# Kernel optimization log

Measured on AMD Instinct MI355X. Metric: run time of the kernel, lower is better.

## Reference

```python
import jax, jax.numpy as jnp
import numpy as np

B, H, S, D = 4, 16, 2048, 64
SQRT_D = float(D) ** 0.5
NEG = -1000000000.0


def setup_inputs() -> dict:
    key = jax.random.key(0)
    kq, kk, kv = jax.random.split(key, 3)
    q = jax.random.normal(kq, (B, H, S, D), dtype=jnp.float32)
    k = jax.random.normal(kk, (B, H, S, D), dtype=jnp.float32)
    v = jax.random.normal(kv, (B, H, S, D), dtype=jnp.float32)
    # causal mask: 1 where attention allowed, 0 where blocked (code masks where mask==0)
    mask = jnp.tril(jnp.ones((S, S), dtype=jnp.int32))[None, None]  # [1,1,S,S]
    return {"q": q, "k": k, "v": v, "mask": mask}


def reference(q, k, v, mask):
    # score: [B,H,S,S]
    score = jnp.einsum("bhqd,bhkd->bhqk", q, k) / SQRT_D
    score = jnp.where(mask == 0, NEG, score)
    attn_weights = jax.nn.softmax(score, axis=-1)
    # dropout p=0.0 -> identity
    attention_output = jnp.einsum("bhqk,bhkd->bhqd", attn_weights, v)
    return (attention_output, attn_weights)
```

## Files before the change

### kernel.cpp

```cpp
#include <hip/hip_runtime.h>
#include <hip/hip_bf16.h>

#define B_ 4
#define H_ 16
#define S_ 2048
#define D_ 64
#define QBLK 128
#define NQB 16
#define THREADS 512

typedef float  f32x4  __attribute__((ext_vector_type(4)));
typedef short  bf16x8 __attribute__((ext_vector_type(8)));
typedef unsigned uint2v __attribute__((ext_vector_type(2)));

#define LOG2E_O8  0.18033688011112042f
#define M20LOG2E -28.853900817779268f

__device__ __forceinline__ unsigned cvt_pk(float lo, float hi) {
    unsigned r;
    asm("v_cvt_pk_bf16_f32 %0, %1, %2" : "=v"(r) : "v"(lo), "v"(hi));
    return r;
}

__device__ __forceinline__ void nt_store4(float* p, f32x4 v) {
    __builtin_nontemporal_store(v, (f32x4*)p);
}

__device__ __forceinline__ void bar_lds() {
    asm volatile("s_waitcnt lgkmcnt(0)\n\ts_barrier" ::: "memory");
}

__device__ __forceinline__ int swz(int row, int s8) {
    return row * 8 + (s8 ^ ((row & 7) ^ ((row >> 3) & 7)));
}

__device__ __forceinline__ bf16x8 frag_ld(const short* lds, int row, int s8) {
    return *(const bf16x8*)((const char*)lds + 16 * swz(row, s8));
}

__device__ __forceinline__ void kload(f32x4 (&r)[2], const float* __restrict__ g, int t) {
    r[0] = *(const f32x4*)(g + 4 * t);
    r[1] = *(const f32x4*)(g + 4 * (t + THREADS));
}
__device__ __forceinline__ void kwrite(short* lds, const f32x4 (&r)[2], int t) {
#pragma unroll
    for (int i = 0; i < 2; ++i) {
        int f = t + i * THREADS;
        int row = f >> 4, c4 = f & 15;
        uint2v h;
        h.x = cvt_pk(r[i].x, r[i].y);
        h.y = cvt_pk(r[i].z, r[i].w);
        *(uint2v*)((char*)lds + 16 * swz(row, c4 >> 1) + (c4 & 1) * 8) = h;
    }
}
__device__ __forceinline__ void vload(f32x4 (&r)[2], const float* __restrict__ g, int t) {
    int k0 = (t >> 4) * 2, d0 = (t & 15) * 4;
    r[0] = *(const f32x4*)(g + k0 * 64 + d0);
    r[1] = *(const f32x4*)(g + (k0 + 1) * 64 + d0);
}
__device__ __forceinline__ void vtwrite(short* lds, const f32x4 (&r)[2], int t) {
    int k0 = (t >> 4) * 2, d0 = (t & 15) * 4;
#pragma unroll
    for (int j = 0; j < 4; ++j) {
        unsigned pk = cvt_pk(r[0][j], r[1][j]);
        int row = d0 + j;
        *(unsigned*)((char*)lds + 16 * swz(row, k0 >> 3) + (k0 & 7) * 2) = pk;
    }
}

__global__ __launch_bounds__(THREADS)
void attn_kernel(const float* __restrict__ Q, const float* __restrict__ K,
                 const float* __restrict__ V, float* __restrict__ Out) {
    const int t    = threadIdx.x;
    const int lane = t & 63;
    const int w    = t >> 6;
    const int l15  = lane & 15;
    const int l4   = lane >> 4;

    const int bid = blockIdx.x;
    const int u   = bid >> 3;
    const int qbi = (NQB - 1) - ((u + 4 * (u >> 5)) & (NQB - 1));
    const int bh  = (bid & 7) * 8 + (u >> 4);
    const int q0  = qbi * QBLK;

    const float* Qg = Q + ((size_t)bh * S_ + q0) * D_;
    const float* Kg = K + (size_t)bh * S_ * D_;
    const float* Vg = V + (size_t)bh * S_ * D_;
    float* Og = Out + ((size_t)bh * S_ + q0) * D_;
    float* Wg = Out + (size_t)B_ * H_ * S_ * D_ + ((size_t)bh * S_ + q0) * (size_t)S_;

    __shared__ char pool[40960];
    short* lkb = (short*)pool;
    short* lv  = (short*)(pool + 16384);
    short* lp  = (short*)(pool + 24576) + w * 1024;

    {
        f32x4 z = {0.f, 0.f, 0.f, 0.f};
        for (int row = 0; row < QBLK; ++row) {
            int c0 = q0 + (row & ~63) + 64;
            float* p = Wg + (size_t)row * S_;
            for (int c = c0 + 4 * t; c < S_; c += 4 * THREADS)
                nt_store4(p + c, z);
        }
    }

    bf16x8 qa0, qa1;
    {
        const float* qrow = Qg + (size_t)(16 * w + l15) * D_;
        f32x4 a0 = *(const f32x4*)(qrow + 8 * l4);
        f32x4 a1 = *(const f32x4*)(qrow + 8 * l4 + 4);
        f32x4 b0 = *(const f32x4*)(qrow + 32 + 8 * l4);
        f32x4 b1 = *(const f32x4*)(qrow + 32 + 8 * l4 + 4);
        union { bf16x8 v; unsigned u[4]; } q0u, q1u;
        q0u.u[0] = cvt_pk(a0.x, a0.y); q0u.u[1] = cvt_pk(a0.z, a0.w);
        q0u.u[2] = cvt_pk(a1.x, a1.y); q0u.u[3] = cvt_pk(a1.z, a1.w);
        q1u.u[0] = cvt_pk(b0.x, b0.y); q1u.u[1] = cvt_pk(b0.z, b0.w);
        q1u.u[2] = cvt_pk(b1.x, b1.y); q1u.u[3] = cvt_pk(b1.z, b1.w);
        qa0 = q0u.v; qa1 = q1u.v;
    }

    const int ktmax  = (q0 + QBLK - 1) >> 6;
    const int qwbase = q0 + 16 * w;
    const int qg     = qwbase + l15;

    f32x4 kreg[2];
    kload(kreg, Kg, t);
    kwrite(lkb, kreg, t);
    kload(kreg, Kg + 4096, t);
    bar_lds();

    f32x4 lsum4 = {0.f, 0.f, 0.f, 0.f};
    for (int kt = 0; kt <= ktmax; ++kt) {
        const short* lk = lkb + (kt & 1) * 4096;
#pragma unroll
        for (int kc = 0; kc < 4; ++kc) {
            int kgb = kt * 64 + 16 * kc;
            if (kgb > qwbase) break;
            bf16x8 kb0 = frag_ld(lk, 16 * kc + l15, 0 + l4);
            bf16x8 kb1 = frag_ld(lk, 16 * kc + l15, 4 + l4);
            f32x4 acc = {0.f, 0.f, 0.f, 0.f};
            acc = __builtin_amdgcn_mfma_f32_16x16x32_bf16(kb0, qa0, acc, 0, 0, 0);
            acc = __builtin_amdgcn_mfma_f32_16x16x32_bf16(kb1, qa1, acc, 0, 0, 0);
            if (kgb != qwbase) {
#pragma unroll
                for (int r = 0; r < 4; ++r)
                    lsum4[r] += exp2f(fmaf(acc[r], LOG2E_O8, M20LOG2E));
            } else {
#pragma unroll
                for (int r = 0; r < 4; ++r) {
                    int kg = kgb + 4 * l4 + r;
                    if (kg <= qg) lsum4[r] += exp2f(fmaf(acc[r], LOG2E_O8, M20LOG2E));
                }
            }
        }
        if (kt < ktmax) {
            kwrite(lkb + ((kt + 1) & 1) * 4096, kreg, t);
            if (kt + 1 < ktmax) kload(kreg, Kg + (size_t)(kt + 2) * 4096, t);
        }
        bar_lds();
    }
    float lsum = (lsum4[0] + lsum4[1]) + (lsum4[2] + lsum4[3]);
    lsum += __shfl_xor(lsum, 16);
    lsum += __shfl_xor(lsum, 32);
    const float c2 = M20LOG2E - __log2f(lsum);

    f32x4 oacc[4];
#pragma unroll
    for (int dt = 0; dt < 4; ++dt) oacc[dt] = (f32x4){0.f, 0.f, 0.f, 0.f};

    f32x4 vreg[2];
    kload(kreg, Kg, t);
    vload(vreg, Vg, t);
    kwrite(lkb, kreg, t);
    vtwrite(lv, vreg, t);
    kload(kreg, Kg + 4096, t);
    vload(vreg, Vg + 4096, t);
    bar_lds();

    for (int kt = 0; kt <= ktmax; ++kt) {
        const short* lk = lkb + (kt & 1) * 4096;
        const bool blive = (kt * 64 <= qwbase);

        if (blive) {
#pragma unroll
            for (int kc = 0; kc < 4; ++kc) {
                int kgb = kt * 64 + 16 * kc;
                bool live = (kgb <= qwbase);
                f32x4 wv;
                if (live) {
                    bf16x8 kb0 = frag_ld(lk, 16 * kc + l15, 0 + l4);
                    bf16x8 kb1 = frag_ld(lk, 16 * kc + l15, 4 + l4);
                    f32x4 acc = {0.f, 0.f, 0.f, 0.f};
                    acc = __builtin_amdgcn_mfma_f32_16x16x32_bf16(kb0, qa0, acc, 0, 0, 0);
                    acc = __builtin_amdgcn_mfma_f32_16x16x32_bf16(kb1, qa1, acc, 0, 0, 0);
                    if (kgb != qwbase) {
#pragma unroll
                        for (int r = 0; r < 4; ++r)
                            wv[r] = exp2f(fmaf(acc[r], LOG2E_O8, c2));
                    } else {
#pragma unroll
                        for (int r = 0; r < 4; ++r) {
                            int kg = kgb + 4 * l4 + r;
                            wv[r] = (kg <= qg) ? exp2f(fmaf(acc[r], LOG2E_O8, c2)) : 0.0f;
                        }
                    }
                } else {
                    wv = (f32x4){0.f, 0.f, 0.f, 0.f};
                }
                uint2v pk;
                pk.x = cvt_pk(wv[0], wv[1]);
                pk.y = cvt_pk(wv[2], wv[3]);
                int s8 = 2 * kc + (l4 >> 1);
                *(uint2v*)((char*)lp + 16 * swz(l15, s8) + (l4 & 1) * 8) = pk;
            }
#pragma unroll
            for (int j = 0; j < 4; ++j) {
                int rr = j * 4 + l4;
                uint2v pk = *(const uint2v*)((char*)lp + 16 * swz(rr, l15 >> 1) + (l15 & 1) * 8);
                f32x4 wf;
                wf.x = __uint_as_float(pk.x << 16);
                wf.y = __uint_as_float(pk.x & 0xffff0000u);
                wf.z = __uint_as_float(pk.y << 16);
                wf.w = __uint_as_float(pk.y & 0xffff0000u);
                nt_store4(Wg + (size_t)(16 * w + rr) * S_ + kt * 64 + 4 * l15, wf);
            }
        }

        if (kt < ktmax) {
            kwrite(lkb + ((kt + 1) & 1) * 4096, kreg, t);
            if (kt + 1 < ktmax) kload(kreg, Kg + (size_t)(kt + 2) * 4096, t);
        }

        if (blive) {
#pragma unroll
            for (int kchunk = 0; kchunk < 2; ++kchunk) {
                bf16x8 pa = frag_ld(lp, l15, kchunk * 4 + l4);
#pragma unroll
                for (int dt = 0; dt < 4; ++dt) {
                    bf16x8 vb = frag_ld(lv, 16 * dt + l15, kchunk * 4 + l4);
                    oacc[dt] = __builtin_amdgcn_mfma_f32_16x16x32_bf16(pa, vb, oacc[dt], 0, 0, 0);
                }
            }
        }
        bar_lds();
        if (kt < ktmax) {
            vtwrite(lv, vreg, t);
            if (kt + 1 < ktmax) vload(vreg, Vg + (size_t)(kt + 2) * 4096, t);
        }
        bar_lds();
    }

#pragma unroll
    for (int dt = 0; dt < 4; ++dt)
#pragma unroll
        for (int r = 0; r < 4; ++r)
            Og[(size_t)(16 * w + 4 * l4 + r) * D_ + 16 * dt + l15] = oacc[dt][r];
}

extern "C" void kernel_launch(void* const* d_in, const int* in_sizes, int n_in,
                              void* d_out, int out_size, void* d_ws, size_t ws_size,
                              hipStream_t stream) {
    const float* q = (const float*)d_in[0];
    const float* k = (const float*)d_in[1];
    const float* v = (const float*)d_in[2];
    float* out = (float*)d_out;
    attn_kernel<<<dim3(B_ * H_ * NQB), dim3(THREADS), 0, stream>>>(q, k, v, out);
}
```

Baseline: 257.9 us.

## Pair complementary causal query tiles per block and interleave zero-fill stores

Each block now handles two 64-row query tiles, a and 31-a, one per group of four waves, so every block carries the same causal workload and the triangular imbalance across blocks goes away. The up-front zero-fill of the masked upper region of the attention-weight matrix is replaced by a quota of zero stores spread over the first-pass key-tile iterations, so those writes overlap with compute. The cost is that the low tile's waves sit through b+1 iterations with most of them idle, and there is more address arithmetic in the fill loop.

```diff
diff --git a/kernel.cpp b/kernel.cpp
--- a/kernel.cpp
+++ b/kernel.cpp
@@ -5,8 +5,6 @@
 #define H_ 16
 #define S_ 2048
 #define D_ 64
-#define QBLK 128
-#define NQB 16
 #define THREADS 512
 
 typedef float  f32x4  __attribute__((ext_vector_type(4)));
@@ -74,39 +72,31 @@
     const int t    = threadIdx.x;
     const int lane = t & 63;
     const int w    = t >> 6;
+    const int wg   = w & 3;
+    const int grp  = w >> 2;
     const int l15  = lane & 15;
     const int l4   = lane >> 4;
 
     const int bid = blockIdx.x;
     const int u   = bid >> 3;
-    const int qbi = (NQB - 1) - ((u + 4 * (u >> 5)) & (NQB - 1));
     const int bh  = (bid & 7) * 8 + (u >> 4);
-    const int q0  = qbi * QBLK;
-
-    const float* Qg = Q + ((size_t)bh * S_ + q0) * D_;
+    const int a   = u & 15;
+    const int b   = 31 - a;
+    const int q0  = (grp ? b : a) * 64;
+
     const float* Kg = K + (size_t)bh * S_ * D_;
     const float* Vg = V + (size_t)bh * S_ * D_;
-    float* Og = Out + ((size_t)bh * S_ + q0) * D_;
-    float* Wg = Out + (size_t)B_ * H_ * S_ * D_ + ((size_t)bh * S_ + q0) * (size_t)S_;
+    float* Wh = Out + (size_t)B_ * H_ * S_ * D_ + (size_t)bh * S_ * (size_t)S_;
+    float* Oh = Out + (size_t)bh * S_ * D_;
 
     __shared__ char pool[40960];
     short* lkb = (short*)pool;
     short* lv  = (short*)(pool + 16384);
     short* lp  = (short*)(pool + 24576) + w * 1024;
 
-    {
-        f32x4 z = {0.f, 0.f, 0.f, 0.f};
-        for (int row = 0; row < QBLK; ++row) {
-            int c0 = q0 + (row & ~63) + 64;
-            float* p = Wg + (size_t)row * S_;
-            for (int c = c0 + 4 * t; c < S_; c += 4 * THREADS)
-                nt_store4(p + c, z);
-        }
-    }
-
     bf16x8 qa0, qa1;
     {
-        const float* qrow = Qg + (size_t)(16 * w + l15) * D_;
+        const float* qrow = Q + ((size_t)bh * S_ + q0 + 16 * wg + l15) * D_;
         f32x4 a0 = *(const f32x4*)(qrow + 8 * l4);
         f32x4 a1 = *(const f32x4*)(qrow + 8 * l4 + 4);
         f32x4 b0 = *(const f32x4*)(qrow + 32 + 8 * l4);
@@ -119,8 +109,7 @@
         qa0 = q0u.v; qa1 = q1u.v;
     }
 
-    const int ktmax  = (q0 + QBLK - 1) >> 6;
-    const int qwbase = q0 + 16 * w;
+    const int qwbase = q0 + 16 * wg;
     const int qg     = qwbase + l15;
 
     f32x4 kreg[2];
@@ -129,33 +118,49 @@
     kload(kreg, Kg + 4096, t);
     bar_lds();
 
+    int fcur = 0;
+    const int fquota = (62 + b) / (b + 1);
+    const f32x4 z4 = {0.f, 0.f, 0.f, 0.f};
+    const int frow = t >> 4, fcol = 4 * (t & 15);
+
     f32x4 lsum4 = {0.f, 0.f, 0.f, 0.f};
-    for (int kt = 0; kt <= ktmax; ++kt) {
+    for (int kt = 0; kt <= b; ++kt) {
         const short* lk = lkb + (kt & 1) * 4096;
-#pragma unroll
-        for (int kc = 0; kc < 4; ++kc) {
-            int kgb = kt * 64 + 16 * kc;
-            if (kgb > qwbase) break;
-            bf16x8 kb0 = frag_ld(lk, 16 * kc + l15, 0 + l4);
-            bf16x8 kb1 = frag_ld(lk, 16 * kc + l15, 4 + l4);
-            f32x4 acc = {0.f, 0.f, 0.f, 0.f};
-            acc = __builtin_amdgcn_mfma_f32_16x16x32_bf16(kb0, qa0, acc, 0, 0, 0);
-            acc = __builtin_amdgcn_mfma_f32_16x16x32_bf16(kb1, qa1, acc, 0, 0, 0);
-            if (kgb != qwbase) {
-#pragma unroll
-                for (int r = 0; r < 4; ++r)
-                    lsum4[r] += exp2f(fmaf(acc[r], LOG2E_O8, M20LOG2E));
-            } else {
-#pragma unroll
-                for (int r = 0; r < 4; ++r) {
-                    int kg = kgb + 4 * l4 + r;
-                    if (kg <= qg) lsum4[r] += exp2f(fmaf(acc[r], LOG2E_O8, M20LOG2E));
+        if (kt * 64 <= qwbase) {
+#pragma unroll
+            for (int kc = 0; kc < 4; ++kc) {
+                int kgb = kt * 64 + 16 * kc;
+                if (kgb > qwbase) break;
+                bf16x8 kb0 = frag_ld(lk, 16 * kc + l15, 0 + l4);
+                bf16x8 kb1 = frag_ld(lk, 16 * kc + l15, 4 + l4);
+                f32x4 acc = {0.f, 0.f, 0.f, 0.f};
+                acc = __builtin_amdgcn_mfma_f32_16x16x32_bf16(kb0, qa0, acc, 0, 0, 0);
+                acc = __builtin_amdgcn_mfma_f32_16x16x32_bf16(kb1, qa1, acc, 0, 0, 0);
+                if (kgb != qwbase) {
+#pragma unroll
+                    for (int r = 0; r < 4; ++r)
+                        lsum4[r] += exp2f(fmaf(acc[r], LOG2E_O8, M20LOG2E));
+                } else {
+#pragma unroll
+                    for (int r = 0; r < 4; ++r) {
+                        int kg = kgb + 4 * l4 + r;
+                        if (kg <= qg) lsum4[r] += exp2f(fmaf(acc[r], LOG2E_O8, M20LOG2E));
+                    }
                 }
             }
         }
-        if (kt < ktmax) {
+        for (int f = 0; f < fquota; ++f) {
+            if (fcur >= 62) break;
+            int zt = fcur >> 1, half = fcur & 1;
+            int rowb, ktile;
+            if (zt < b) { rowb = 64 * a; ktile = a + 1 + zt; }
+            else        { rowb = 64 * b; ktile = zt + 1; }
+            nt_store4(Wh + (size_t)(rowb + 32 * half + frow) * S_ + 64 * ktile + fcol, z4);
+            ++fcur;
+        }
+        if (kt < b) {
             kwrite(lkb + ((kt + 1) & 1) * 4096, kreg, t);
-            if (kt + 1 < ktmax) kload(kreg, Kg + (size_t)(kt + 2) * 4096, t);
+            if (kt + 1 < b) kload(kreg, Kg + (size_t)(kt + 2) * 4096, t);
         }
         bar_lds();
     }
@@ -177,7 +182,7 @@
     vload(vreg, Vg + 4096, t);
     bar_lds();
 
-    for (int kt = 0; kt <= ktmax; ++kt) {
+    for (int kt = 0; kt <= b; ++kt) {
         const short* lk = lkb + (kt & 1) * 4096;
         const bool blive = (kt * 64 <= qwbase);
 
@@ -222,13 +227,13 @@
                 wf.y = __uint_as_float(pk.x & 0xffff0000u);
                 wf.z = __uint_as_float(pk.y << 16);
                 wf.w = __uint_as_float(pk.y & 0xffff0000u);
-                nt_store4(Wg + (size_t)(16 * w + rr) * S_ + kt * 64 + 4 * l15, wf);
-            }
-        }
-
-        if (kt < ktmax) {
+                nt_store4(Wh + (size_t)(qwbase + rr) * S_ + kt * 64 + 4 * l15, wf);
+            }
+        }
+
+        if (kt < b) {
             kwrite(lkb + ((kt + 1) & 1) * 4096, kreg, t);
-            if (kt + 1 < ktmax) kload(kreg, Kg + (size_t)(kt + 2) * 4096, t);
+            if (kt + 1 < b) kload(kreg, Kg + (size_t)(kt + 2) * 4096, t);
         }
 
         if (blive) {
@@ -243,9 +248,9 @@
             }
         }
         bar_lds();
-        if (kt < ktmax) {
+        if (kt < b) {
             vtwrite(lv, vreg, t);
-            if (kt + 1 < ktmax) vload(vreg, Vg + (size_t)(kt + 2) * 4096, t);
+            if (kt + 1 < b) vload(vreg, Vg + (size_t)(kt + 2) * 4096, t);
         }
         bar_lds();
     }
@@ -254,7 +259,7 @@
     for (int dt = 0; dt < 4; ++dt)
 #pragma unroll
         for (int r = 0; r < 4; ++r)
-            Og[(size_t)(16 * w + 4 * l4 + r) * D_ + 16 * dt + l15] = oacc[dt][r];
+            Oh[(size_t)(qwbase + 4 * l4 + r) * D_ + 16 * dt + l15] = oacc[dt][r];
 }
 
 extern "C" void kernel_launch(void* const* d_in, const int* in_sizes, int n_in,
@@ -264,5 +269,5 @@
     const float* k = (const float*)d_in[1];
     const float* v = (const float*)d_in[2];
     float* out = (float*)d_out;
-    attn_kernel<<<dim3(B_ * H_ * NQB), dim3(THREADS), 0, stream>>>(q, k, v, out);
-}
+    attn_kernel<<<dim3(1024), dim3(THREADS), 0, stream>>>(q, k, v, out);
+}
```

Result: faster. 241.4 us (-6.4%).
